# Performance work log

Measured on AMD Instinct MI355X. Metric: run time of the kernel, lower is better.

## Reference

```python
import jax, jax.numpy as jnp
import numpy as np

B, S, D, DFF = 4, 2048, 1024, 4096
EPS = 1e-5


def layernorm(x, gamma, beta):
    mu = jnp.mean(x, axis=-1, keepdims=True)
    var = jnp.var(x, axis=-1, keepdims=True)
    return (x - mu) * jax.lax.rsqrt(var + EPS) * gamma + beta


def attention(Q, K, V, causal):
    d_k = Q.shape[-1]
    scores = jnp.einsum('bqd,bkd->bqk', Q, K) / jnp.sqrt(jnp.asarray(d_k, Q.dtype))
    if causal:
        q_len, k_len = scores.shape[-2], scores.shape[-1]
        mask = jnp.tril(jnp.ones((q_len, k_len), dtype=bool))
        scores = jnp.where(mask[None], scores, jnp.asarray(-jnp.inf, scores.dtype))
    w = jax.nn.softmax(scores, axis=-1)
    return jnp.einsum('bqk,bkd->bqd', w, V)


def setup_inputs() -> dict:
    key = jax.random.key(0)
    ks = jax.random.split(key, 12)
    sd = 0.02
    return {
        'y': jax.random.normal(ks[0], (B, S, D), jnp.float32),
        'Z': jax.random.normal(ks[1], (B, S, D), jnp.float32),
        'w1': jax.random.normal(ks[2], (D, DFF), jnp.float32) * sd,
        'b1': jnp.zeros((DFF,), jnp.float32),
        'w2': jax.random.normal(ks[3], (DFF, D), jnp.float32) * sd,
        'b2': jnp.zeros((D,), jnp.float32),
        'g1': jnp.ones((D,), jnp.float32), 'beta1': jnp.zeros((D,), jnp.float32),
        'g2': jnp.ones((D,), jnp.float32), 'beta2': jnp.zeros((D,), jnp.float32),
        'g3': jnp.ones((D,), jnp.float32), 'beta3': jnp.zeros((D,), jnp.float32),
    }


def reference(y, Z, w1, b1, w2, b2, g1, beta1, g2, beta2, g3, beta3):
    # masked (causal) self-attention, single head over full d_model
    sa = attention(y, y, y, causal=True)
    y = layernorm(y + sa, g1, beta1)
    # cross-attention to encoder memory Z
    ca = attention(y, Z, Z, causal=False)
    y = layernorm(y + ca, g2, beta2)
    # position-wise FFN
    h = jax.nn.relu(jnp.einsum('bsd,df->bsf', y, w1) + b1)
    ff = jnp.einsum('bsf,fd->bsd', h, w2) + b2
    y = layernorm(y + ff, g3, beta3)
    return y
```

## Files before the change

### kernel.cpp

```cpp
#include <hip/hip_runtime.h>
#include <hip/hip_bf16.h>


#define Bb 4
#define Ss 2048
#define Dd 1024
#define Ff 4096

typedef __attribute__((ext_vector_type(4))) float f32x4;
typedef __attribute__((ext_vector_type(8))) short bf16x8;
typedef __attribute__((ext_vector_type(8))) unsigned short u16x8;
typedef __attribute__((ext_vector_type(4))) unsigned short u16x4;

__device__ __forceinline__ unsigned short f2bf(float f) {
  unsigned u = __float_as_uint(f);
  u += 0x7FFFu + ((u >> 16) & 1u);
  return (unsigned short)(u >> 16);
}

__device__ __forceinline__ void gload_lds16(const void* g, void* l) {
  __builtin_amdgcn_global_load_lds((const __attribute__((address_space(1))) void*)g,
                                   (__attribute__((address_space(3))) void*)l, 16, 0, 0);
}

__device__ __forceinline__ int xcd8(int orig, int n) {
  int q = n >> 3, r = n & 7;
  int x = orig & 7;
  int base = x < r ? x * (q + 1) : r * (q + 1) + (x - r) * q;
  return base + (orig >> 3);
}

__global__ __launch_bounds__(256) void k_transpose_cast(const float* __restrict__ in,
                                                        unsigned short* __restrict__ outT,
                                                        unsigned short* __restrict__ outR,
                                                        int R, int C) {
  __shared__ float t[32][33];
  size_t bo = (size_t)blockIdx.z * R * C;
  const float* pin = in + bo;
  unsigned short* poutT = outT + bo;
  unsigned short* poutR = outR ? outR + bo : nullptr;
  int c0 = blockIdx.x * 32, r0 = blockIdx.y * 32;
  int tx = threadIdx.x, ty = threadIdx.y;
#pragma unroll
  for (int i = 0; i < 4; i++) {
    float v = pin[(size_t)(r0 + ty + i * 8) * C + c0 + tx];
    t[ty + i * 8][tx] = v;
    if (poutR) poutR[(size_t)(r0 + ty + i * 8) * C + c0 + tx] = f2bf(v);
  }
  __syncthreads();
#pragma unroll
  for (int i = 0; i < 4; i++)
    poutT[(size_t)(c0 + ty + i * 8) * R + r0 + tx] = f2bf(t[tx][ty + i * 8]);
}

#define BAR() __builtin_amdgcn_s_barrier()
#define PRIO1() __builtin_amdgcn_s_setprio(1)
#define PRIO0() __builtin_amdgcn_s_setprio(0)

#define LDA8(arr, mh, bo)                                                       \
  {                                                                             \
    _Pragma("unroll") for (int j_ = 0; j_ < QM; ++j_) {                         \
      _Pragma("unroll") for (int kh_ = 0; kh_ < 2; ++kh_) {                     \
        arr[j_][kh_] =                                                          \
            *(const bf16x8*)(lds + (bo) + ((mh)*QM + j_) * 2048 + aof[kh_]);    \
      }                                                                         \
    }                                                                           \
  }

#define LDB8(arr, nh, bo)                                                       \
  {                                                                             \
    _Pragma("unroll") for (int n_ = 0; n_ < 2; ++n_) {                          \
      _Pragma("unroll") for (int kh_ = 0; kh_ < 2; ++kh_) {                     \
        arr[n_][kh_] =                                                          \
            *(const bf16x8*)(lds + (bo) + ((nh)*2 + n_) * 2048 + bof[kh_]);     \
      }                                                                         \
    }                                                                           \
  }

#define MMQ(aarr, barr, mh, nh)                                                 \
  {                                                                             \
    _Pragma("unroll") for (int j_ = 0; j_ < QM; ++j_) {                         \
      _Pragma("unroll") for (int n_ = 0; n_ < 2; ++n_) {                        \
        _Pragma("unroll") for (int kh_ = 0; kh_ < 2; ++kh_) {                   \
          acc[(mh)*QM + j_][(nh)*2 + n_] = __builtin_amdgcn_mfma_f32_16x16x32_bf16( \
              aarr[j_][kh_], barr[n_][kh_], acc[(mh)*QM + j_][(nh)*2 + n_], 0, 0, 0); \
        }                                                                       \
      }                                                                         \
    }                                                                           \
  }

#define VMCNT()                                                                 \
  {                                                                             \
    if constexpr (NVM == 6) asm volatile("s_waitcnt vmcnt(6)" ::: "memory");    \
    else asm volatile("s_waitcnt vmcnt(4)" ::: "memory");                       \
  }

template <int BMt, int EPI, bool CAUSAL, bool KCAP>
__global__ __launch_bounds__(512) void k_gemm8(
    const unsigned short* __restrict__ Ag, const unsigned short* __restrict__ Bg,
    float* __restrict__ Cf, unsigned short* __restrict__ Cb,
    const float* __restrict__ bias, int K, int lda, int ldb, int ldc,
    long bsA, long bsB, long bsC, float scale) {
  constexpr int BNt = 256;
  constexpr int WMS = BMt / 2;
  constexpr int MR = WMS / 16;
  constexpr int QM = MR / 2;
  constexpr int LA = BMt / 128;
  constexpr int NVM = 2 * LA + 2;
  constexpr int ABYTES = BMt * 128;
  constexpr int BBYTES = BNt * 128;
  __shared__ alignas(16) char lds[2 * ABYTES + 2 * BBYTES];

  int i0, j0;
  if (CAUSAL) {
    int t = xcd8(blockIdx.x, gridDim.x);
    int ti = (int)((sqrtf(8.f * t + 1.f) - 1.f) * 0.5f);
    while ((ti + 1) * (ti + 2) / 2 <= t) ++ti;
    while (ti * (ti + 1) / 2 > t) --ti;
    i0 = ti * BMt;
    j0 = (t - ti * (ti + 1) / 2) * BNt;
  } else {
    int lin = xcd8(blockIdx.y * gridDim.x + blockIdx.x, gridDim.x * gridDim.y);
    i0 = (lin / gridDim.x) * BMt;
    j0 = (lin % gridDim.x) * BNt;
  }
  int bz = blockIdx.z;
  Ag += (size_t)bz * bsA;
  Bg += (size_t)bz * bsB;

  int nk = K / 64;
  if (KCAP) {
    int cap = i0 / 64 + BMt / 64;
    nk = nk < cap ? nk : cap;
  }
  const int niter = nk / 2;

  const int tid = threadIdx.x;
  const int w = tid >> 6, lane = tid & 63;
  const int wr = w >> 2, wc = w & 3;

  const int srow = (w << 3) + (lane >> 3);
  const int bcs = (lane & 7) ^ (lane >> 3);
  const unsigned short* As = Ag + (size_t)(i0 + srow) * lda + bcs * 8;
  const unsigned short* Bs = Bg + (size_t)(j0 + srow) * ldb + bcs * 8;
  char* ldsAw = lds + w * 1024;
  char* ldsBw = lds + 2 * ABYTES + w * 1024;

  auto stA = [&](int kt, int hf) {
    int ks = kt < nk ? kt : nk - 1;
#pragma unroll
    for (int l = 0; l < LA; ++l)
      gload_lds16(As + (size_t)(hf * (BMt / 2) + l * 64) * lda + ks * 64,
                  ldsAw + (kt & 1) * ABYTES + hf * (BMt / 2) * 128 + l * 8192);
  };
  auto stB = [&](int kt, int hf) {
    int ks = kt < nk ? kt : nk - 1;
#pragma unroll
    for (int l = 0; l < 2; ++l)
      gload_lds16(Bs + (size_t)(hf * 128 + l * 64) * ldb + ks * 64,
                  ldsBw + (kt & 1) * BBYTES + hf * 128 * 128 + l * 8192);
  };

  const int fr = lane & 15, kq = lane >> 4;
  const int rA = wr * WMS + fr;
  const int rB = wc * 64 + fr;
  unsigned aof[2], bof[2];
  aof[0] = rA * 128 + ((kq ^ (rA & 7)) << 4);
  aof[1] = rA * 128 + (((kq + 4) ^ (rA & 7)) << 4);
  bof[0] = 2 * ABYTES + rB * 128 + ((kq ^ (rB & 7)) << 4);
  bof[1] = 2 * ABYTES + rB * 128 + (((kq + 4) ^ (rB & 7)) << 4);
  constexpr int A0 = 0, A1 = ABYTES, B0 = 0, B1 = BBYTES;

  f32x4 acc[MR][4];
#pragma unroll
  for (int m = 0; m < MR; ++m)
#pragma unroll
    for (int n = 0; n < 4; ++n) acc[m][n] = (f32x4){0.f, 0.f, 0.f, 0.f};

  bf16x8 a0[QM][2], a1[QM][2], b0[2][2], b1[2][2];

  stA(0, 0); stA(0, 1); stB(0, 0); stB(0, 1);
  stA(1, 0); stA(1, 1); stB(1, 0);
  VMCNT();
  BAR();

  for (int t = 0; t < niter; ++t) {
    const int ka = 2 * t + 2, kb = 2 * t + 3;
    LDA8(a0, 0, A0); LDB8(b0, 0, B0);
    stB(2 * t + 1, 1);
    BAR(); PRIO1(); MMQ(a0, b0, 0, 0); PRIO0(); BAR();
    LDA8(a1, 1, A0);
    BAR(); PRIO1(); MMQ(a1, b0, 1, 0); PRIO0(); BAR();
    LDB8(b1, 1, B0);
    stA(ka, 0);
    BAR(); PRIO1(); MMQ(a1, b1, 1, 1); PRIO0(); BAR();
    stA(ka, 1); stB(ka, 0);
    VMCNT();
    BAR(); PRIO1(); MMQ(a0, b1, 0, 1); PRIO0(); BAR();
    LDA8(a0, 0, A1); LDB8(b0, 0, B1);
    stB(ka, 1);
    BAR(); PRIO1(); MMQ(a0, b0, 0, 0); PRIO0(); BAR();
    LDA8(a1, 1, A1);
    BAR(); PRIO1(); MMQ(a1, b0, 1, 0); PRIO0(); BAR();
    LDB8(b1, 1, B1);
    stA(kb, 0);
    BAR(); PRIO1(); MMQ(a1, b1, 1, 1); PRIO0(); BAR();
    stA(kb, 1); stB(kb, 0);
    VMCNT();
    BAR(); PRIO1(); MMQ(a0, b1, 0, 1); PRIO0(); BAR();
  }

  const int colb = j0 + wc * 64 + fr;
  const int rowb = i0 + wr * WMS + (kq << 2);
  const size_t cb = (size_t)bz * bsC;
#pragma unroll
  for (int m = 0; m < MR; ++m) {
#pragma unroll
    for (int r = 0; r < 4; ++r) {
      size_t ro = cb + (size_t)(rowb + m * 16 + r) * ldc;
#pragma unroll
      for (int n = 0; n < 4; ++n) {
        float v = acc[m][n][r];
        int col = colb + n * 16;
        if (EPI == 0) Cf[ro + col] = v * scale;
        else if (EPI == 1) Cf[ro + col] = v;
        else if (EPI == 2) Cb[ro + col] = f2bf(fmaxf(v + bias[col], 0.f));
        else Cf[ro + col] = v + bias[col];
      }
    }
  }
}

template <bool CAUSAL>
__global__ __launch_bounds__(256) void k_softmax(float* __restrict__ scores) {
  int row = blockIdx.x;
  int i = row & (Ss - 1);
  float* src = scores + (size_t)row * Ss;
  unsigned short* dst = (unsigned short*)src;
  int nv = CAUSAL ? i + 1 : Ss;
  int t = threadIdx.x;
  int w = t >> 6, lane = t & 63;
  float v[8];
  float mx = -1e30f;
#pragma unroll
  for (int k = 0; k < 8; k++) {
    int j = t + k * 256;
    v[k] = (j < nv) ? src[j] : -1e30f;
    mx = fmaxf(mx, v[k]);
  }
#pragma unroll
  for (int o = 32; o; o >>= 1) mx = fmaxf(mx, __shfl_xor(mx, o));
  __shared__ float red[8];
  if (lane == 0) red[w] = mx;
  __syncthreads();
  mx = fmaxf(fmaxf(red[0], red[1]), fmaxf(red[2], red[3]));
  float sum = 0.f;
#pragma unroll
  for (int k = 0; k < 8; k++) {
    int j = t + k * 256;
    float e = (j < nv) ? __expf(v[k] - mx) : 0.f;
    v[k] = e;
    sum += e;
  }
#pragma unroll
  for (int o = 32; o; o >>= 1) sum += __shfl_xor(sum, o);
  if (lane == 0) red[4 + w] = sum;
  __syncthreads();
  sum = red[4] + red[5] + red[6] + red[7];
  float inv = 1.f / sum;
#pragma unroll
  for (int k = 0; k < 8; k++) {
    int j = t + k * 256;
    dst[j] = f2bf(v[k] * inv);
  }
}

__global__ __launch_bounds__(256) void k_add_ln(const float* __restrict__ a,
                                                const float* __restrict__ b,
                                                const float* __restrict__ g,
                                                const float* __restrict__ be,
                                                float* __restrict__ outf,
                                                unsigned short* __restrict__ outb) {
  int row = blockIdx.x;
  size_t o = (size_t)row * Dd;
  int t = threadIdx.x;
  f32x4 xa = *(const f32x4*)(a + o + t * 4);
  f32x4 xb = *(const f32x4*)(b + o + t * 4);
  f32x4 x = xa + xb;
  float s = x[0] + x[1] + x[2] + x[3];
  float q = x[0] * x[0] + x[1] * x[1] + x[2] * x[2] + x[3] * x[3];
  int w = t >> 6, lane = t & 63;
#pragma unroll
  for (int of = 32; of; of >>= 1) {
    s += __shfl_xor(s, of);
    q += __shfl_xor(q, of);
  }
  __shared__ float red[8];
  if (lane == 0) {
    red[w] = s;
    red[4 + w] = q;
  }
  __syncthreads();
  s = red[0] + red[1] + red[2] + red[3];
  q = red[4] + red[5] + red[6] + red[7];
  float mean = s * (1.f / Dd);
  float var = q * (1.f / Dd) - mean * mean;
  float rstd = rsqrtf(var + 1e-5f);
  f32x4 gv = *(const f32x4*)(g + t * 4);
  f32x4 bv = *(const f32x4*)(be + t * 4);
  f32x4 y;
#pragma unroll
  for (int k = 0; k < 4; k++) y[k] = (x[k] - mean) * rstd * gv[k] + bv[k];
  *(f32x4*)(outf + o + t * 4) = y;
  if (outb) {
    u16x4 r;
    r[0] = f2bf(y[0]); r[1] = f2bf(y[1]); r[2] = f2bf(y[2]); r[3] = f2bf(y[3]);
    *(u16x4*)(outb + o + t * 4) = r;
  }
}

extern "C" void kernel_launch(void* const* d_in, const int* in_sizes, int n_in, void* d_out,
                              int out_size, void* d_ws, size_t ws_size, hipStream_t stream) {
  (void)in_sizes; (void)n_in; (void)out_size; (void)ws_size;
  const float* y   = (const float*)d_in[0];
  const float* Z   = (const float*)d_in[1];
  const float* w1  = (const float*)d_in[2];
  const float* b1  = (const float*)d_in[3];
  const float* w2  = (const float*)d_in[4];
  const float* b2  = (const float*)d_in[5];
  const float* g1  = (const float*)d_in[6];
  const float* be1 = (const float*)d_in[7];
  const float* g2  = (const float*)d_in[8];
  const float* be2 = (const float*)d_in[9];
  const float* g3  = (const float*)d_in[10];
  const float* be3 = (const float*)d_in[11];
  float* out = (float*)d_out;

  char* ws = (char*)d_ws;
  const size_t MB = 1024ull * 1024ull;
  unsigned short* T   = (unsigned short*)(ws);
  unsigned short* Zbf = (unsigned short*)(ws + 16 * MB);
  unsigned short* ybf = (unsigned short*)(ws + 32 * MB);
  unsigned short* w1t = (unsigned short*)(ws + 48 * MB);
  unsigned short* w2t = (unsigned short*)(ws + 56 * MB);
  float* sc           = (float*)(ws + 64 * MB);
  unsigned short* h   = (unsigned short*)(ws + 64 * MB);
  float* res          = (float*)(ws + 128 * MB);
  float* attn         = (float*)d_out;

  dim3 b256(256), b512(512);
  const float scl = 1.f / 32.f;

  k_transpose_cast<<<dim3(Dd / 32, Ss / 32, Bb), dim3(32, 8), 0, stream>>>(y, T, ybf, Ss, Dd);
  k_gemm8<256, 0, true, false><<<dim3(36, 1, Bb), b512, 0, stream>>>(
      ybf, ybf, sc, nullptr, nullptr, Dd, Dd, Dd, Ss, (long)Ss * Dd, (long)Ss * Dd,
      (long)Ss * Ss, scl);
  k_softmax<true><<<dim3(Bb * Ss), b256, 0, stream>>>(sc);
  k_gemm8<128, 1, false, true><<<dim3(Dd / 256, Ss / 128, Bb), b512, 0, stream>>>(
      (const unsigned short*)sc, T, attn, nullptr, nullptr, Ss, 2 * Ss, Ss, Dd,
      2L * Ss * Ss, (long)Dd * Ss, (long)Ss * Dd, 1.f);
  k_add_ln<<<dim3(Bb * Ss), b256, 0, stream>>>(y, attn, g1, be1, res, ybf);

  k_transpose_cast<<<dim3(Dd / 32, Ss / 32, Bb), dim3(32, 8), 0, stream>>>(Z, T, Zbf, Ss, Dd);
  k_gemm8<256, 0, false, false><<<dim3(Ss / 256, Ss / 256, Bb), b512, 0, stream>>>(
      ybf, Zbf, sc, nullptr, nullptr, Dd, Dd, Dd, Ss, (long)Ss * Dd, (long)Ss * Dd,
      (long)Ss * Ss, scl);
  k_softmax<false><<<dim3(Bb * Ss), b256, 0, stream>>>(sc);
  k_gemm8<128, 1, false, false><<<dim3(Dd / 256, Ss / 128, Bb), b512, 0, stream>>>(
      (const unsigned short*)sc, T, attn, nullptr, nullptr, Ss, 2 * Ss, Ss, Dd,
      2L * Ss * Ss, (long)Dd * Ss, (long)Ss * Dd, 1.f);
  k_add_ln<<<dim3(Bb * Ss), b256, 0, stream>>>(res, attn, g2, be2, res, ybf);

  k_transpose_cast<<<dim3(Ff / 32, Dd / 32, 1), dim3(32, 8), 0, stream>>>(w1, w1t, nullptr, Dd, Ff);
  k_transpose_cast<<<dim3(Dd / 32, Ff / 32, 1), dim3(32, 8), 0, stream>>>(w2, w2t, nullptr, Ff, Dd);
  k_gemm8<256, 2, false, false><<<dim3(Ff / 256, (Bb * Ss) / 256, 1), b512, 0, stream>>>(
      ybf, w1t, nullptr, h, b1, Dd, Dd, Dd, Ff, 0L, 0L, 0L, 1.f);
  k_gemm8<128, 3, false, false><<<dim3(Dd / 256, (Bb * Ss) / 128, 1), b512, 0, stream>>>(
      h, w2t, attn, nullptr, b2, Ff, Ff, Ff, Dd, 0L, 0L, 0L, 1.f);
  k_add_ln<<<dim3(Bb * Ss), b256, 0, stream>>>(res, attn, g3, be3, out, nullptr);
}
```

Before: 406.5 us.

## Replace 512-thread GEMM with simpler 256x128 kernel, bf16 scores, fused residual

Replaces the hand-scheduled 512-thread, K=64 ping-pong GEMM with a simpler 256-thread, 256x128-tile, K=32 double-buffered kernel that runs at up to 3 blocks per CU. Attention scores are now written directly as bf16 by the GEMM epilogue, so the softmax reads half the bytes and skips fully masked causal blocks. The residual add moves into the GEMM epilogue, which turns add+layernorm into a plain layernorm. The price is the loss of the fine-grained MFMA/load interleaving and a barrier on every K step, plus somewhat lower precision because scores are rounded to bf16 before softmax.

```diff
diff --git a/kernel.cpp b/kernel.cpp
--- a/kernel.cpp
+++ b/kernel.cpp
@@ -16,6 +16,9 @@
   unsigned u = __float_as_uint(f);
   u += 0x7FFFu + ((u >> 16) & 1u);
   return (unsigned short)(u >> 16);
+}
+__device__ __forceinline__ float bf2f(unsigned short h) {
+  return __uint_as_float(((unsigned)h) << 16);
 }
 
 __device__ __forceinline__ void gload_lds16(const void* g, void* l) {
@@ -53,168 +56,101 @@
     poutT[(size_t)(c0 + ty + i * 8) * R + r0 + tx] = f2bf(t[tx][ty + i * 8]);
 }
 
-#define BAR() __builtin_amdgcn_s_barrier()
 #define PRIO1() __builtin_amdgcn_s_setprio(1)
 #define PRIO0() __builtin_amdgcn_s_setprio(0)
 
-#define LDA8(arr, mh, bo)                                                       \
-  {                                                                             \
-    _Pragma("unroll") for (int j_ = 0; j_ < QM; ++j_) {                         \
-      _Pragma("unroll") for (int kh_ = 0; kh_ < 2; ++kh_) {                     \
-        arr[j_][kh_] =                                                          \
-            *(const bf16x8*)(lds + (bo) + ((mh)*QM + j_) * 2048 + aof[kh_]);    \
-      }                                                                         \
-    }                                                                           \
-  }
-
-#define LDB8(arr, nh, bo)                                                       \
-  {                                                                             \
-    _Pragma("unroll") for (int n_ = 0; n_ < 2; ++n_) {                          \
-      _Pragma("unroll") for (int kh_ = 0; kh_ < 2; ++kh_) {                     \
-        arr[n_][kh_] =                                                          \
-            *(const bf16x8*)(lds + (bo) + ((nh)*2 + n_) * 2048 + bof[kh_]);     \
-      }                                                                         \
-    }                                                                           \
-  }
-
-#define MMQ(aarr, barr, mh, nh)                                                 \
-  {                                                                             \
-    _Pragma("unroll") for (int j_ = 0; j_ < QM; ++j_) {                         \
-      _Pragma("unroll") for (int n_ = 0; n_ < 2; ++n_) {                        \
-        _Pragma("unroll") for (int kh_ = 0; kh_ < 2; ++kh_) {                   \
-          acc[(mh)*QM + j_][(nh)*2 + n_] = __builtin_amdgcn_mfma_f32_16x16x32_bf16( \
-              aarr[j_][kh_], barr[n_][kh_], acc[(mh)*QM + j_][(nh)*2 + n_], 0, 0, 0); \
-        }                                                                       \
-      }                                                                         \
-    }                                                                           \
-  }
-
-#define VMCNT()                                                                 \
-  {                                                                             \
-    if constexpr (NVM == 6) asm volatile("s_waitcnt vmcnt(6)" ::: "memory");    \
-    else asm volatile("s_waitcnt vmcnt(4)" ::: "memory");                       \
-  }
-
-template <int BMt, int EPI, bool CAUSAL, bool KCAP>
-__global__ __launch_bounds__(512) void k_gemm8(
+template <int EPI, bool CAUSAL, bool KCAP>
+__global__ __launch_bounds__(256, 3) void k_gemmW(
     const unsigned short* __restrict__ Ag, const unsigned short* __restrict__ Bg,
     float* __restrict__ Cf, unsigned short* __restrict__ Cb,
-    const float* __restrict__ bias, int K, int lda, int ldb, int ldc,
-    long bsA, long bsB, long bsC, float scale) {
-  constexpr int BNt = 256;
-  constexpr int WMS = BMt / 2;
-  constexpr int MR = WMS / 16;
-  constexpr int QM = MR / 2;
-  constexpr int LA = BMt / 128;
-  constexpr int NVM = 2 * LA + 2;
-  constexpr int ABYTES = BMt * 128;
-  constexpr int BBYTES = BNt * 128;
-  __shared__ alignas(16) char lds[2 * ABYTES + 2 * BBYTES];
+    const float* __restrict__ bias, const float* __restrict__ resid,
+    int K, int lda, int ldb, int ldc, long bsA, long bsB, long bsC, float scale) {
+  constexpr int ABY = 256 * 64;
+  constexpr int BBY = 128 * 64;
+  __shared__ alignas(16) char lds[2 * ABY + 2 * BBY];
 
   int i0, j0;
   if (CAUSAL) {
     int t = xcd8(blockIdx.x, gridDim.x);
-    int ti = (int)((sqrtf(8.f * t + 1.f) - 1.f) * 0.5f);
-    while ((ti + 1) * (ti + 2) / 2 <= t) ++ti;
-    while (ti * (ti + 1) / 2 > t) --ti;
-    i0 = ti * BMt;
-    j0 = (t - ti * (ti + 1) / 2) * BNt;
+    int ti = (int)((sqrtf(4.f * t + 1.f) - 1.f) * 0.5f);
+    while ((ti + 1) * (ti + 2) <= t) ++ti;
+    while (ti * (ti + 1) > t) --ti;
+    i0 = ti * 256;
+    j0 = (t - ti * (ti + 1)) * 128;
   } else {
     int lin = xcd8(blockIdx.y * gridDim.x + blockIdx.x, gridDim.x * gridDim.y);
-    i0 = (lin / gridDim.x) * BMt;
-    j0 = (lin % gridDim.x) * BNt;
+    i0 = (lin / gridDim.x) * 256;
+    j0 = (lin % gridDim.x) * 128;
   }
   int bz = blockIdx.z;
   Ag += (size_t)bz * bsA;
   Bg += (size_t)bz * bsB;
 
-  int nk = K / 64;
+  int nk = K / 32;
   if (KCAP) {
-    int cap = i0 / 64 + BMt / 64;
+    int cap = i0 / 32 + 8;
     nk = nk < cap ? nk : cap;
   }
-  const int niter = nk / 2;
 
   const int tid = threadIdx.x;
   const int w = tid >> 6, lane = tid & 63;
-  const int wr = w >> 2, wc = w & 3;
-
-  const int srow = (w << 3) + (lane >> 3);
-  const int bcs = (lane & 7) ^ (lane >> 3);
-  const unsigned short* As = Ag + (size_t)(i0 + srow) * lda + bcs * 8;
-  const unsigned short* Bs = Bg + (size_t)(j0 + srow) * ldb + bcs * 8;
-  char* ldsAw = lds + w * 1024;
-  char* ldsBw = lds + 2 * ABYTES + w * 1024;
-
-  auto stA = [&](int kt, int hf) {
+  const int wr = w >> 1, wc = w & 1;
+
+  const int tr = tid >> 2, tc = tid & 3;
+  const int scs = tc ^ (tr & 3);
+  const unsigned short* As = Ag + (size_t)(i0 + tr) * lda + scs * 8;
+  const unsigned short* Bs = Bg + (size_t)(j0 + tr) * ldb + scs * 8;
+  char* ldsA = lds + tid * 16;
+  char* ldsB = lds + 2 * ABY + tid * 16;
+
+  auto stage = [&](int kt) {
     int ks = kt < nk ? kt : nk - 1;
-#pragma unroll
-    for (int l = 0; l < LA; ++l)
-      gload_lds16(As + (size_t)(hf * (BMt / 2) + l * 64) * lda + ks * 64,
-                  ldsAw + (kt & 1) * ABYTES + hf * (BMt / 2) * 128 + l * 8192);
+    int boA = (kt & 1) * ABY, boB = (kt & 1) * BBY;
+#pragma unroll
+    for (int i = 0; i < 4; ++i)
+      gload_lds16(As + (size_t)(i * 64) * lda + ks * 32, ldsA + boA + i * 4096);
+#pragma unroll
+    for (int i = 0; i < 2; ++i)
+      gload_lds16(Bs + (size_t)(i * 64) * ldb + ks * 32, ldsB + boB + i * 4096);
   };
-  auto stB = [&](int kt, int hf) {
-    int ks = kt < nk ? kt : nk - 1;
-#pragma unroll
-    for (int l = 0; l < 2; ++l)
-      gload_lds16(Bs + (size_t)(hf * 128 + l * 64) * ldb + ks * 64,
-                  ldsBw + (kt & 1) * BBYTES + hf * 128 * 128 + l * 8192);
-  };
 
   const int fr = lane & 15, kq = lane >> 4;
-  const int rA = wr * WMS + fr;
+  const int rA = wr * 128 + fr;
   const int rB = wc * 64 + fr;
-  unsigned aof[2], bof[2];
-  aof[0] = rA * 128 + ((kq ^ (rA & 7)) << 4);
-  aof[1] = rA * 128 + (((kq + 4) ^ (rA & 7)) << 4);
-  bof[0] = 2 * ABYTES + rB * 128 + ((kq ^ (rB & 7)) << 4);
-  bof[1] = 2 * ABYTES + rB * 128 + (((kq + 4) ^ (rB & 7)) << 4);
-  constexpr int A0 = 0, A1 = ABYTES, B0 = 0, B1 = BBYTES;
-
-  f32x4 acc[MR][4];
-#pragma unroll
-  for (int m = 0; m < MR; ++m)
+  const unsigned aof = rA * 64 + ((kq ^ (rA & 3)) << 4);
+  const unsigned bof = rB * 64 + ((kq ^ (rB & 3)) << 4);
+
+  f32x4 acc[8][4];
+#pragma unroll
+  for (int m = 0; m < 8; ++m)
 #pragma unroll
     for (int n = 0; n < 4; ++n) acc[m][n] = (f32x4){0.f, 0.f, 0.f, 0.f};
 
-  bf16x8 a0[QM][2], a1[QM][2], b0[2][2], b1[2][2];
-
-  stA(0, 0); stA(0, 1); stB(0, 0); stB(0, 1);
-  stA(1, 0); stA(1, 1); stB(1, 0);
-  VMCNT();
-  BAR();
-
-  for (int t = 0; t < niter; ++t) {
-    const int ka = 2 * t + 2, kb = 2 * t + 3;
-    LDA8(a0, 0, A0); LDB8(b0, 0, B0);
-    stB(2 * t + 1, 1);
-    BAR(); PRIO1(); MMQ(a0, b0, 0, 0); PRIO0(); BAR();
-    LDA8(a1, 1, A0);
-    BAR(); PRIO1(); MMQ(a1, b0, 1, 0); PRIO0(); BAR();
-    LDB8(b1, 1, B0);
-    stA(ka, 0);
-    BAR(); PRIO1(); MMQ(a1, b1, 1, 1); PRIO0(); BAR();
-    stA(ka, 1); stB(ka, 0);
-    VMCNT();
-    BAR(); PRIO1(); MMQ(a0, b1, 0, 1); PRIO0(); BAR();
-    LDA8(a0, 0, A1); LDB8(b0, 0, B1);
-    stB(ka, 1);
-    BAR(); PRIO1(); MMQ(a0, b0, 0, 0); PRIO0(); BAR();
-    LDA8(a1, 1, A1);
-    BAR(); PRIO1(); MMQ(a1, b0, 1, 0); PRIO0(); BAR();
-    LDB8(b1, 1, B1);
-    stA(kb, 0);
-    BAR(); PRIO1(); MMQ(a1, b1, 1, 1); PRIO0(); BAR();
-    stA(kb, 1); stB(kb, 0);
-    VMCNT();
-    BAR(); PRIO1(); MMQ(a0, b1, 0, 1); PRIO0(); BAR();
+  stage(0);
+  for (int kt = 0; kt < nk; ++kt) {
+    __syncthreads();
+    if (kt + 1 < nk) stage(kt + 1);
+    const char* pA = lds + (kt & 1) * ABY + aof;
+    const char* pB = lds + 2 * ABY + (kt & 1) * BBY + bof;
+    bf16x8 a[8], b[4];
+#pragma unroll
+    for (int mi = 0; mi < 8; ++mi) a[mi] = *(const bf16x8*)(pA + mi * 1024);
+#pragma unroll
+    for (int ni = 0; ni < 4; ++ni) b[ni] = *(const bf16x8*)(pB + ni * 1024);
+    PRIO1();
+#pragma unroll
+    for (int mi = 0; mi < 8; ++mi)
+#pragma unroll
+      for (int ni = 0; ni < 4; ++ni)
+        acc[mi][ni] = __builtin_amdgcn_mfma_f32_16x16x32_bf16(a[mi], b[ni], acc[mi][ni], 0, 0, 0);
+    PRIO0();
   }
 
   const int colb = j0 + wc * 64 + fr;
-  const int rowb = i0 + wr * WMS + (kq << 2);
+  const int rowb = i0 + wr * 128 + (kq << 2);
   const size_t cb = (size_t)bz * bsC;
 #pragma unroll
-  for (int m = 0; m < MR; ++m) {
+  for (int m = 0; m < 8; ++m) {
 #pragma unroll
     for (int r = 0; r < 4; ++r) {
       size_t ro = cb + (size_t)(rowb + m * 16 + r) * ldc;
@@ -222,31 +158,38 @@
       for (int n = 0; n < 4; ++n) {
         float v = acc[m][n][r];
         int col = colb + n * 16;
-        if (EPI == 0) Cf[ro + col] = v * scale;
-        else if (EPI == 1) Cf[ro + col] = v;
+        if (EPI == 0) Cb[ro + col] = f2bf(v * scale);
         else if (EPI == 2) Cb[ro + col] = f2bf(fmaxf(v + bias[col], 0.f));
-        else Cf[ro + col] = v + bias[col];
+        else if (EPI == 4) Cf[ro + col] = v + resid[ro + col];
+        else Cf[ro + col] = v + bias[col] + resid[ro + col];
       }
     }
   }
 }
 
 template <bool CAUSAL>
-__global__ __launch_bounds__(256) void k_softmax(float* __restrict__ scores) {
+__global__ __launch_bounds__(256) void k_softmax(unsigned short* __restrict__ scores) {
   int row = blockIdx.x;
   int i = row & (Ss - 1);
-  float* src = scores + (size_t)row * Ss;
-  unsigned short* dst = (unsigned short*)src;
+  unsigned short* src = scores + (size_t)row * Ss;
   int nv = CAUSAL ? i + 1 : Ss;
+  int nb = CAUSAL ? ((i & ~255) + 256) : Ss;
   int t = threadIdx.x;
   int w = t >> 6, lane = t & 63;
+  bool act = t * 8 < nb;
   float v[8];
   float mx = -1e30f;
-#pragma unroll
-  for (int k = 0; k < 8; k++) {
-    int j = t + k * 256;
-    v[k] = (j < nv) ? src[j] : -1e30f;
-    mx = fmaxf(mx, v[k]);
+  if (act) {
+    u16x8 raw = *(const u16x8*)(src + t * 8);
+#pragma unroll
+    for (int k = 0; k < 8; k++) {
+      int j = t * 8 + k;
+      v[k] = (j < nv) ? bf2f(raw[k]) : -1e30f;
+      mx = fmaxf(mx, v[k]);
+    }
+  } else {
+#pragma unroll
+    for (int k = 0; k < 8; k++) v[k] = -1e30f;
   }
 #pragma unroll
   for (int o = 32; o; o >>= 1) mx = fmaxf(mx, __shfl_xor(mx, o));
@@ -257,8 +200,7 @@
   float sum = 0.f;
 #pragma unroll
   for (int k = 0; k < 8; k++) {
-    int j = t + k * 256;
-    float e = (j < nv) ? __expf(v[k] - mx) : 0.f;
+    float e = (v[k] > -1e29f) ? __expf(v[k] - mx) : 0.f;
     v[k] = e;
     sum += e;
   }
@@ -268,25 +210,23 @@
   __syncthreads();
   sum = red[4] + red[5] + red[6] + red[7];
   float inv = 1.f / sum;
-#pragma unroll
-  for (int k = 0; k < 8; k++) {
-    int j = t + k * 256;
-    dst[j] = f2bf(v[k] * inv);
-  }
-}
-
-__global__ __launch_bounds__(256) void k_add_ln(const float* __restrict__ a,
-                                                const float* __restrict__ b,
-                                                const float* __restrict__ g,
-                                                const float* __restrict__ be,
-                                                float* __restrict__ outf,
-                                                unsigned short* __restrict__ outb) {
+  if (act) {
+    u16x8 r;
+#pragma unroll
+    for (int k = 0; k < 8; k++) r[k] = f2bf(v[k] * inv);
+    *(u16x8*)(src + t * 8) = r;
+  }
+}
+
+__global__ __launch_bounds__(256) void k_ln(const float* __restrict__ a,
+                                            const float* __restrict__ g,
+                                            const float* __restrict__ be,
+                                            float* __restrict__ outf,
+                                            unsigned short* __restrict__ outb) {
   int row = blockIdx.x;
   size_t o = (size_t)row * Dd;
   int t = threadIdx.x;
-  f32x4 xa = *(const f32x4*)(a + o + t * 4);
-  f32x4 xb = *(const f32x4*)(b + o + t * 4);
-  f32x4 x = xa + xb;
+  f32x4 x = *(const f32x4*)(a + o + t * 4);
   float s = x[0] + x[1] + x[2] + x[3];
   float q = x[0] * x[0] + x[1] * x[1] + x[2] * x[2] + x[3] * x[3];
   int w = t >> 6, lane = t & 63;
@@ -343,39 +283,36 @@
   unsigned short* ybf = (unsigned short*)(ws + 32 * MB);
   unsigned short* w1t = (unsigned short*)(ws + 48 * MB);
   unsigned short* w2t = (unsigned short*)(ws + 56 * MB);
-  float* sc           = (float*)(ws + 64 * MB);
+  unsigned short* sc  = (unsigned short*)(ws + 64 * MB);
   unsigned short* h   = (unsigned short*)(ws + 64 * MB);
   float* res          = (float*)(ws + 128 * MB);
   float* attn         = (float*)d_out;
 
-  dim3 b256(256), b512(512);
+  dim3 b256(256);
   const float scl = 1.f / 32.f;
+  const long SD = (long)Ss * Dd, SS = (long)Ss * Ss;
 
   k_transpose_cast<<<dim3(Dd / 32, Ss / 32, Bb), dim3(32, 8), 0, stream>>>(y, T, ybf, Ss, Dd);
-  k_gemm8<256, 0, true, false><<<dim3(36, 1, Bb), b512, 0, stream>>>(
-      ybf, ybf, sc, nullptr, nullptr, Dd, Dd, Dd, Ss, (long)Ss * Dd, (long)Ss * Dd,
-      (long)Ss * Ss, scl);
+  k_gemmW<0, true, false><<<dim3(72, 1, Bb), b256, 0, stream>>>(
+      ybf, ybf, nullptr, sc, nullptr, nullptr, Dd, Dd, Dd, Ss, SD, SD, SS, scl);
   k_softmax<true><<<dim3(Bb * Ss), b256, 0, stream>>>(sc);
-  k_gemm8<128, 1, false, true><<<dim3(Dd / 256, Ss / 128, Bb), b512, 0, stream>>>(
-      (const unsigned short*)sc, T, attn, nullptr, nullptr, Ss, 2 * Ss, Ss, Dd,
-      2L * Ss * Ss, (long)Dd * Ss, (long)Ss * Dd, 1.f);
-  k_add_ln<<<dim3(Bb * Ss), b256, 0, stream>>>(y, attn, g1, be1, res, ybf);
+  k_gemmW<4, false, true><<<dim3(Dd / 128, Ss / 256, Bb), b256, 0, stream>>>(
+      sc, T, attn, nullptr, nullptr, y, Ss, Ss, Ss, Dd, SS, SD, SD, 1.f);
+  k_ln<<<dim3(Bb * Ss), b256, 0, stream>>>(attn, g1, be1, res, ybf);
 
   k_transpose_cast<<<dim3(Dd / 32, Ss / 32, Bb), dim3(32, 8), 0, stream>>>(Z, T, Zbf, Ss, Dd);
-  k_gemm8<256, 0, false, false><<<dim3(Ss / 256, Ss / 256, Bb), b512, 0, stream>>>(
-      ybf, Zbf, sc, nullptr, nullptr, Dd, Dd, Dd, Ss, (long)Ss * Dd, (long)Ss * Dd,
-      (long)Ss * Ss, scl);
+  k_gemmW<0, false, false><<<dim3(Ss / 128, Ss / 256, Bb), b256, 0, stream>>>(
+      ybf, Zbf, nullptr, sc, nullptr, nullptr, Dd, Dd, Dd, Ss, SD, SD, SS, scl);
   k_softmax<false><<<dim3(Bb * Ss), b256, 0, stream>>>(sc);
-  k_gemm8<128, 1, false, false><<<dim3(Dd / 256, Ss / 128, Bb), b512, 0, stream>>>(
-      (const unsigned short*)sc, T, attn, nullptr, nullptr, Ss, 2 * Ss, Ss, Dd,
-      2L * Ss * Ss, (long)Dd * Ss, (long)Ss * Dd, 1.f);
-  k_add_ln<<<dim3(Bb * Ss), b256, 0, stream>>>(res, attn, g2, be2, res, ybf);
+  k_gemmW<4, false, false><<<dim3(Dd / 128, Ss / 256, Bb), b256, 0, stream>>>(
+      sc, T, attn, nullptr, nullptr, res, Ss, Ss, Ss, Dd, SS, SD, SD, 1.f);
+  k_ln<<<dim3(Bb * Ss), b256, 0, stream>>>(attn, g2, be2, res, ybf);
 
   k_transpose_cast<<<dim3(Ff / 32, Dd / 32, 1), dim3(32, 8), 0, stream>>>(w1, w1t, nullptr, Dd, Ff);
   k_transpose_cast<<<dim3(Dd / 32, Ff / 32, 1), dim3(32, 8), 0, stream>>>(w2, w2t, nullptr, Ff, Dd);
-  k_gemm8<256, 2, false, false><<<dim3(Ff / 256, (Bb * Ss) / 256, 1), b512, 0, stream>>>(
-      ybf, w1t, nullptr, h, b1, Dd, Dd, Dd, Ff, 0L, 0L, 0L, 1.f);
-  k_gemm8<128, 3, false, false><<<dim3(Dd / 256, (Bb * Ss) / 128, 1), b512, 0, stream>>>(
-      h, w2t, attn, nullptr, b2, Ff, Ff, Ff, Dd, 0L, 0L, 0L, 1.f);
-  k_add_ln<<<dim3(Bb * Ss), b256, 0, stream>>>(res, attn, g3, be3, out, nullptr);
-}
+  k_gemmW<2, false, false><<<dim3(Ff / 128, (Bb * Ss) / 256, 1), b256, 0, stream>>>(
+      ybf, w1t, nullptr, h, b1, nullptr, Dd, Dd, Dd, Ff, 0L, 0L, 0L, 1.f);
+  k_gemmW<5, false, false><<<dim3(Dd / 128, (Bb * Ss) / 256, 1), b256, 0, stream>>>(
+      h, w2t, attn, nullptr, b2, res, Ff, Ff, Ff, Dd, 0L, 0L, 0L, 1.f);
+  k_ln<<<dim3(Bb * Ss), b256, 0, stream>>>(attn, g3, be3, out, nullptr);
+}
```

New measurement: 1.089 ms. +168.0%, slower.
